# Performance work log

Measured on AMD Instinct MI355X. Metric: run time of the kernel, lower is better.

## Reference

```python
import jax, jax.numpy as jnp
import numpy as np

IGNORE_INDEX = -100
N, C = 2097152, 32


def setup_inputs() -> dict:
    key = jax.random.key(0)
    k1, k2, k3 = jax.random.split(key, 3)
    pred = jax.random.normal(k1, (N, C), dtype=jnp.float32)
    # neg_count (~0.95N) > pos_num * factor (~0.15N).
    r = jax.random.randint(k2, (N,), 0, 100, dtype=jnp.int32)
    cls = jax.random.randint(k3, (N,), 1, C, dtype=jnp.int32)
    label = jnp.where(r >= 95, cls, 0).astype(jnp.int32)
    return {"pred": pred, "label": label, "factor": 3}


def reference(pred, label, factor):
    n = pred.shape[0]
    is_pos = label != 0
    pos_num = jnp.sum(is_pos)
    neg_sum = pos_num * factor
    num_neg = n - pos_num

    # max non-background score per row
    pred_value = jnp.max(pred[:, 1:], axis=1)  # [N]

    # descending sort of negative-position scores (positives pushed to the end)
    neg_scores = jnp.where(is_pos, -jnp.inf, pred_value)
    sorted_desc = -jnp.sort(-neg_scores)
    idx = jnp.clip(neg_sum - 1, 0, n - 1)
    threshold = sorted_desc[idx]

    mask_thr = (pred_value >= threshold) | is_pos
    mask_all = label != -1
    mask = jnp.where(num_neg > neg_sum, mask_thr, mask_all)
    mask = jax.lax.stop_gradient(mask)  # torch computes mask on detached numpy

    masked_label = jnp.where(mask, label, IGNORE_INDEX)
    valid = masked_label != IGNORE_INDEX
    safe_label = jnp.where(valid, masked_label, 0)

    logp = jax.nn.log_softmax(pred, axis=-1)  # [N, C]
    nll = -jnp.take_along_axis(logp, safe_label[:, None], axis=1)[:, 0]  # [N]
    denom = jnp.maximum(jnp.sum(valid), 1)
    loss = jnp.sum(jnp.where(valid, nll, 0.0)) / denom.astype(pred.dtype)
    return loss
```

## Files before the change

### kernel.cpp

```cpp
#include <hip/hip_runtime.h>

#define IGNORE_INDEX (-100)
#define C_DIM 32

struct Ctrl {
    unsigned hist[4][256];
    unsigned pos_num;
    unsigned prefix;
    unsigned rank;
    unsigned use_thr;
    unsigned cnt;
    unsigned pad;
    double   sum;
};

__global__ void init_kernel(unsigned* c, int words) {
    for (int i = threadIdx.x + blockIdx.x * blockDim.x; i < words;
         i += blockDim.x * gridDim.x)
        c[i] = 0u;
}

__device__ inline void wave_hist_add(unsigned* h, unsigned bucket) {
    unsigned long long todo = __ballot(1);
    while (todo) {
        int leader = (int)__builtin_ctzll(todo);
        unsigned b = __shfl(bucket, leader);
        unsigned long long same = __ballot(bucket == b) & todo;
        if ((int)(threadIdx.x & 63) == leader)
            atomicAdd(&h[b], (unsigned)__popcll(same));
        todo &= ~same;
    }
}

__global__ void __launch_bounds__(256)
row_kernel(const float* __restrict__ pred, const int* __restrict__ label,
           unsigned* __restrict__ keys, float* __restrict__ nll,
           Ctrl* __restrict__ c, int n) {
    __shared__ unsigned h[256];
    for (int i = threadIdx.x; i < 256; i += 256) h[i] = 0u;
    __syncthreads();

    int pos_local = 0;
    const int stride = gridDim.x * blockDim.x;
    for (int row = blockIdx.x * blockDim.x + threadIdx.x; row < n; row += stride) {
        const float4* p = reinterpret_cast<const float4*>(pred) + (size_t)row * 8;
        float r[32];
#pragma unroll
        for (int j = 0; j < 8; ++j) {
            float4 v = p[j];
            r[4 * j + 0] = v.x; r[4 * j + 1] = v.y;
            r[4 * j + 2] = v.z; r[4 * j + 3] = v.w;
        }
        float m_nb = r[1];
#pragma unroll
        for (int j = 2; j < 32; ++j) m_nb = fmaxf(m_nb, r[j]);
        float m_all = fmaxf(m_nb, r[0]);

        float s = 0.f;
#pragma unroll
        for (int j = 0; j < 32; ++j) s += __expf(r[j] - m_all);

        int lab = label[row];
        int sl = lab; if (sl < 0) sl = 0; if (sl > 31) sl = 31;
        float xl = r[0];
#pragma unroll
        for (int j = 1; j < 32; ++j) xl = (j == sl) ? r[j] : xl;

        nll[row] = (m_all + __logf(s)) - xl;

        bool is_pos = (lab != 0);
        pos_local += is_pos ? 1 : 0;

        float ns = is_pos ? -__builtin_inff() : m_nb;
        unsigned u = __float_as_uint(ns);
        unsigned ukey = (u & 0x80000000u) ? ~u : (u | 0x80000000u);
        unsigned dkey = ~ukey;
        keys[row] = dkey;
        wave_hist_add(h, dkey >> 24);
    }

#pragma unroll
    for (int off = 32; off > 0; off >>= 1) pos_local += __shfl_down(pos_local, off);
    __shared__ int wsum[4];
    int wid = threadIdx.x >> 6, lane = threadIdx.x & 63;
    if (lane == 0) wsum[wid] = pos_local;
    __syncthreads();
    if (threadIdx.x == 0)
        atomicAdd(&c->pos_num, (unsigned)(wsum[0] + wsum[1] + wsum[2] + wsum[3]));

    for (int i = threadIdx.x; i < 256; i += 256)
        if (h[i]) atomicAdd(&c->hist[3][i], h[i]);
}

__global__ void __launch_bounds__(256)
hist_kernel(const unsigned* __restrict__ keys, Ctrl* __restrict__ c, int n, int pass) {
    __shared__ unsigned h[256];
    for (int i = threadIdx.x; i < 256; i += 256) h[i] = 0u;
    __syncthreads();
    const unsigned prefix = c->prefix;
    const unsigned pmask = 0xFFFFFFFFu << (8 * (pass + 1));
    const int shift = 8 * pass;
    const int stride = gridDim.x * blockDim.x;
    for (int i = blockIdx.x * blockDim.x + threadIdx.x; i < n; i += stride) {
        unsigned k = keys[i];
        if ((k & pmask) == prefix) atomicAdd(&h[(k >> shift) & 0xFFu], 1u);
    }
    __syncthreads();
    for (int i = threadIdx.x; i < 256; i += 256)
        if (h[i]) atomicAdd(&c->hist[pass][i], h[i]);
}

__global__ void scan_kernel(Ctrl* __restrict__ c, const int* __restrict__ factor_p,
                            int pass, int n) {
    __shared__ unsigned s[256];
    __shared__ unsigned sh_rank;
    int t = threadIdx.x;
    if (t == 0) {
        if (pass == 3) {
            long long pos = (long long)c->pos_num;
            long long fac = (long long)factor_p[0];
            long long neg_sum = pos * fac;
            long long num_neg = (long long)n - pos;
            long long idx = neg_sum - 1;
            if (idx < 0) idx = 0;
            if (idx > (long long)n - 1) idx = (long long)n - 1;
            sh_rank = (unsigned)idx;
            c->use_thr = (num_neg > neg_sum) ? 1u : 0u;
        } else {
            sh_rank = c->rank;
        }
    }
    __syncthreads();
    unsigned cnt = c->hist[pass][t];
    s[t] = cnt;
    __syncthreads();
#pragma unroll
    for (int off = 1; off < 256; off <<= 1) {
        unsigned v = (t >= off) ? s[t - off] : 0u;
        __syncthreads();
        s[t] += v;
        __syncthreads();
    }
    unsigned rank = sh_rank;
    unsigned incl = s[t];
    unsigned excl = incl - cnt;
    if (cnt > 0u && excl <= rank && rank < incl) {
        c->prefix |= ((unsigned)t) << (8 * pass);
        c->rank = rank - excl;
    }
}

__global__ void __launch_bounds__(256)
reduce_kernel(const unsigned* __restrict__ keys, const int* __restrict__ label,
              const float* __restrict__ nll, Ctrl* __restrict__ c, int n) {
    const bool use_thr = (c->use_thr != 0u);
    const unsigned thr = c->prefix;
    double local = 0.0;
    int cntl = 0;
    const int stride = gridDim.x * blockDim.x;
    for (int i = blockIdx.x * blockDim.x + threadIdx.x; i < n; i += stride) {
        int lab = label[i];
        bool mask = use_thr ? ((lab != 0) || (keys[i] <= thr)) : (lab != -1);
        if (mask) { local += (double)nll[i]; cntl++; }
    }
#pragma unroll
    for (int off = 32; off > 0; off >>= 1) {
        local += __shfl_down(local, off);
        cntl  += __shfl_down(cntl, off);
    }
    __shared__ double sd[4];
    __shared__ int    si[4];
    int wid = threadIdx.x >> 6, lane = threadIdx.x & 63;
    if (lane == 0) { sd[wid] = local; si[wid] = cntl; }
    __syncthreads();
    if (threadIdx.x == 0) {
        double tot = sd[0] + sd[1] + sd[2] + sd[3];
        int ct = si[0] + si[1] + si[2] + si[3];
        atomicAdd(&c->sum, tot);
        atomicAdd(&c->cnt, (unsigned)ct);
    }
}

__global__ void final_kernel(const Ctrl* __restrict__ c, float* __restrict__ out) {
    if (threadIdx.x == 0 && blockIdx.x == 0) {
        unsigned ct = c->cnt;
        double denom = (ct == 0u) ? 1.0 : (double)ct;
        out[0] = (float)(c->sum / denom);
    }
}

extern "C" void kernel_launch(void* const* d_in, const int* in_sizes, int n_in,
                              void* d_out, int out_size, void* d_ws, size_t ws_size,
                              hipStream_t stream) {
    const float* pred  = (const float*)d_in[0];
    const int* label   = (const int*)d_in[1];
    const int* factor  = (const int*)d_in[2];
    int n = in_sizes[1];
    float* out = (float*)d_out;

    char* ws = (char*)d_ws;
    Ctrl* c = (Ctrl*)ws;
    unsigned* keys = (unsigned*)(ws + 8192);
    float* nll = (float*)(ws + 8192 + (size_t)n * sizeof(unsigned));

    init_kernel<<<1, 256, 0, stream>>>((unsigned*)c, (int)(sizeof(Ctrl) / 4));
    row_kernel<<<2048, 256, 0, stream>>>(pred, label, keys, nll, c, n);
    scan_kernel<<<1, 256, 0, stream>>>(c, factor, 3, n);
    hist_kernel<<<1024, 256, 0, stream>>>(keys, c, n, 2);
    scan_kernel<<<1, 256, 0, stream>>>(c, factor, 2, n);
    hist_kernel<<<1024, 256, 0, stream>>>(keys, c, n, 1);
    scan_kernel<<<1, 256, 0, stream>>>(c, factor, 1, n);
    hist_kernel<<<1024, 256, 0, stream>>>(keys, c, n, 0);
    scan_kernel<<<1, 256, 0, stream>>>(c, factor, 0, n);
    reduce_kernel<<<2048, 256, 0, stream>>>(keys, label, nll, c, n);
    final_kernel<<<1, 64, 0, stream>>>(c, out);
}
```

Baseline: 167.3 us.

## Split each row across 8 lanes and fold scan passes into consumer kernels

The row kernel now assigns one float4 per lane, with 8 lanes per row, and uses shuffles for the max, sum-exp and label gather. This gives fully coalesced loads in place of per-thread 128-byte strided row reads, and cuts register pressure. The four single-block scan kernels are removed: every block of the hist and reduce kernels recomputes the radix-select prefix chain from the global histograms, which drops four launches but repeats the scans redundantly in each block. The histogram atomics now run only on one lane in eight, which leaves most lanes idle during that step.

```diff
diff --git a/kernel.cpp b/kernel.cpp
--- a/kernel.cpp
+++ b/kernel.cpp
@@ -1,16 +1,10 @@
 #include <hip/hip_runtime.h>
 
-#define IGNORE_INDEX (-100)
-#define C_DIM 32
 
 struct Ctrl {
     unsigned hist[4][256];
     unsigned pos_num;
-    unsigned prefix;
-    unsigned rank;
-    unsigned use_thr;
     unsigned cnt;
-    unsigned pad;
     double   sum;
 };
 
@@ -33,57 +27,61 @@
 }
 
 __global__ void __launch_bounds__(256)
-row_kernel(const float* __restrict__ pred, const int* __restrict__ label,
+row_kernel(const float4* __restrict__ pred4, const int* __restrict__ label,
            unsigned* __restrict__ keys, float* __restrict__ nll,
            Ctrl* __restrict__ c, int n) {
     __shared__ unsigned h[256];
     for (int i = threadIdx.x; i < 256; i += 256) h[i] = 0u;
     __syncthreads();
 
+    const int lane  = threadIdx.x & 63;
+    const int sub   = lane & 7;
+    const int gbase = lane & ~7;
+
     int pos_local = 0;
-    const int stride = gridDim.x * blockDim.x;
-    for (int row = blockIdx.x * blockDim.x + threadIdx.x; row < n; row += stride) {
-        const float4* p = reinterpret_cast<const float4*>(pred) + (size_t)row * 8;
-        float r[32];
-#pragma unroll
-        for (int j = 0; j < 8; ++j) {
-            float4 v = p[j];
-            r[4 * j + 0] = v.x; r[4 * j + 1] = v.y;
-            r[4 * j + 2] = v.z; r[4 * j + 3] = v.w;
+    const int rows_per_iter = (gridDim.x * blockDim.x) >> 3;
+    for (int row = (int)((blockIdx.x * blockDim.x + threadIdx.x) >> 3);
+         row < n; row += rows_per_iter) {
+        float4 v = pred4[(size_t)row * 8 + sub];
+
+        float m_nb = (sub == 0) ? fmaxf(fmaxf(v.y, v.z), v.w)
+                                : fmaxf(fmaxf(v.x, v.y), fmaxf(v.z, v.w));
+        m_nb = fmaxf(m_nb, __shfl_xor(m_nb, 1));
+        m_nb = fmaxf(m_nb, __shfl_xor(m_nb, 2));
+        m_nb = fmaxf(m_nb, __shfl_xor(m_nb, 4));
+        float r0    = __shfl(v.x, gbase);
+        float m_all = fmaxf(m_nb, r0);
+
+        float s = __expf(v.x - m_all) + __expf(v.y - m_all)
+                + __expf(v.z - m_all) + __expf(v.w - m_all);
+        s += __shfl_xor(s, 1);
+        s += __shfl_xor(s, 2);
+        s += __shfl_xor(s, 4);
+
+        int lab = label[row];
+        int sl = lab; sl = sl < 0 ? 0 : sl; sl = sl > 31 ? 31 : sl;
+        float cand = (sl & 2) ? ((sl & 1) ? v.w : v.z)
+                              : ((sl & 1) ? v.y : v.x);
+        float xl = __shfl(cand, gbase | (sl >> 2));
+
+        if (sub == 0) {
+            nll[row] = (m_all + __logf(s)) - xl;
+            bool is_pos = (lab != 0);
+            pos_local += is_pos ? 1 : 0;
+            float ns = is_pos ? -__builtin_inff() : m_nb;
+            unsigned u    = __float_as_uint(ns);
+            unsigned ukey = (u & 0x80000000u) ? ~u : (u | 0x80000000u);
+            unsigned dkey = ~ukey;
+            keys[row] = dkey;
+            wave_hist_add(h, dkey >> 24);
         }
-        float m_nb = r[1];
-#pragma unroll
-        for (int j = 2; j < 32; ++j) m_nb = fmaxf(m_nb, r[j]);
-        float m_all = fmaxf(m_nb, r[0]);
-
-        float s = 0.f;
-#pragma unroll
-        for (int j = 0; j < 32; ++j) s += __expf(r[j] - m_all);
-
-        int lab = label[row];
-        int sl = lab; if (sl < 0) sl = 0; if (sl > 31) sl = 31;
-        float xl = r[0];
-#pragma unroll
-        for (int j = 1; j < 32; ++j) xl = (j == sl) ? r[j] : xl;
-
-        nll[row] = (m_all + __logf(s)) - xl;
-
-        bool is_pos = (lab != 0);
-        pos_local += is_pos ? 1 : 0;
-
-        float ns = is_pos ? -__builtin_inff() : m_nb;
-        unsigned u = __float_as_uint(ns);
-        unsigned ukey = (u & 0x80000000u) ? ~u : (u | 0x80000000u);
-        unsigned dkey = ~ukey;
-        keys[row] = dkey;
-        wave_hist_add(h, dkey >> 24);
     }
 
 #pragma unroll
     for (int off = 32; off > 0; off >>= 1) pos_local += __shfl_down(pos_local, off);
     __shared__ int wsum[4];
-    int wid = threadIdx.x >> 6, lane = threadIdx.x & 63;
-    if (lane == 0) wsum[wid] = pos_local;
+    int wid = threadIdx.x >> 6;
+    if ((threadIdx.x & 63) == 0) wsum[wid] = pos_local;
     __syncthreads();
     if (threadIdx.x == 0)
         atomicAdd(&c->pos_num, (unsigned)(wsum[0] + wsum[1] + wsum[2] + wsum[3]));
@@ -92,12 +90,59 @@
         if (h[i]) atomicAdd(&c->hist[3][i], h[i]);
 }
 
+__device__ void select_chain(const Ctrl* __restrict__ c, int n, int factor,
+                             int upto_pass, unsigned& prefix_out,
+                             unsigned& rank_out, bool& use_thr_out) {
+    __shared__ unsigned s[256];
+    __shared__ unsigned sh_byte, sh_rank;
+    const int t = threadIdx.x;
+
+    long long pos     = (long long)c->pos_num;
+    long long neg_sum = pos * (long long)factor;
+    long long num_neg = (long long)n - pos;
+    long long idx     = neg_sum - 1;
+    if (idx < 0) idx = 0;
+    if (idx > (long long)n - 1) idx = (long long)n - 1;
+    unsigned rank   = (unsigned)idx;
+    unsigned prefix = 0u;
+
+    for (int p = 3; p >= upto_pass; --p) {
+        unsigned cnt = c->hist[p][t];
+        __syncthreads();
+        s[t] = cnt;
+        __syncthreads();
+#pragma unroll
+        for (int off = 1; off < 256; off <<= 1) {
+            unsigned v = (t >= off) ? s[t - off] : 0u;
+            __syncthreads();
+            s[t] += v;
+            __syncthreads();
+        }
+        unsigned incl = s[t], excl = incl - cnt;
+        if (cnt > 0u && excl <= rank && rank < incl) {
+            sh_byte = (unsigned)t;
+            sh_rank = rank - excl;
+        }
+        __syncthreads();
+        prefix |= sh_byte << (8 * p);
+        rank = sh_rank;
+        __syncthreads();
+    }
+    prefix_out  = prefix;
+    rank_out    = rank;
+    use_thr_out = (num_neg > neg_sum);
+}
+
 __global__ void __launch_bounds__(256)
-hist_kernel(const unsigned* __restrict__ keys, Ctrl* __restrict__ c, int n, int pass) {
+hist_kernel(const unsigned* __restrict__ keys, Ctrl* __restrict__ c,
+            const int* __restrict__ factor_p, int n, int pass) {
+    unsigned prefix, rank; bool use_thr;
+    select_chain(c, n, factor_p[0], pass + 1, prefix, rank, use_thr);
+
     __shared__ unsigned h[256];
     for (int i = threadIdx.x; i < 256; i += 256) h[i] = 0u;
     __syncthreads();
-    const unsigned prefix = c->prefix;
+
     const unsigned pmask = 0xFFFFFFFFu << (8 * (pass + 1));
     const int shift = 8 * pass;
     const int stride = gridDim.x * blockDim.x;
@@ -110,51 +155,13 @@
         if (h[i]) atomicAdd(&c->hist[pass][i], h[i]);
 }
 
-__global__ void scan_kernel(Ctrl* __restrict__ c, const int* __restrict__ factor_p,
-                            int pass, int n) {
-    __shared__ unsigned s[256];
-    __shared__ unsigned sh_rank;
-    int t = threadIdx.x;
-    if (t == 0) {
-        if (pass == 3) {
-            long long pos = (long long)c->pos_num;
-            long long fac = (long long)factor_p[0];
-            long long neg_sum = pos * fac;
-            long long num_neg = (long long)n - pos;
-            long long idx = neg_sum - 1;
-            if (idx < 0) idx = 0;
-            if (idx > (long long)n - 1) idx = (long long)n - 1;
-            sh_rank = (unsigned)idx;
-            c->use_thr = (num_neg > neg_sum) ? 1u : 0u;
-        } else {
-            sh_rank = c->rank;
-        }
-    }
-    __syncthreads();
-    unsigned cnt = c->hist[pass][t];
-    s[t] = cnt;
-    __syncthreads();
-#pragma unroll
-    for (int off = 1; off < 256; off <<= 1) {
-        unsigned v = (t >= off) ? s[t - off] : 0u;
-        __syncthreads();
-        s[t] += v;
-        __syncthreads();
-    }
-    unsigned rank = sh_rank;
-    unsigned incl = s[t];
-    unsigned excl = incl - cnt;
-    if (cnt > 0u && excl <= rank && rank < incl) {
-        c->prefix |= ((unsigned)t) << (8 * pass);
-        c->rank = rank - excl;
-    }
-}
-
 __global__ void __launch_bounds__(256)
 reduce_kernel(const unsigned* __restrict__ keys, const int* __restrict__ label,
-              const float* __restrict__ nll, Ctrl* __restrict__ c, int n) {
-    const bool use_thr = (c->use_thr != 0u);
-    const unsigned thr = c->prefix;
+              const float* __restrict__ nll, Ctrl* __restrict__ c,
+              const int* __restrict__ factor_p, int n) {
+    unsigned thr, rank; bool use_thr;
+    select_chain(c, n, factor_p[0], 0, thr, rank, use_thr);
+
     double local = 0.0;
     int cntl = 0;
     const int stride = gridDim.x * blockDim.x;
@@ -170,14 +177,12 @@
     }
     __shared__ double sd[4];
     __shared__ int    si[4];
-    int wid = threadIdx.x >> 6, lane = threadIdx.x & 63;
-    if (lane == 0) { sd[wid] = local; si[wid] = cntl; }
+    int wid = threadIdx.x >> 6;
+    if ((threadIdx.x & 63) == 0) { sd[wid] = local; si[wid] = cntl; }
     __syncthreads();
     if (threadIdx.x == 0) {
-        double tot = sd[0] + sd[1] + sd[2] + sd[3];
-        int ct = si[0] + si[1] + si[2] + si[3];
-        atomicAdd(&c->sum, tot);
-        atomicAdd(&c->cnt, (unsigned)ct);
+        atomicAdd(&c->sum, sd[0] + sd[1] + sd[2] + sd[3]);
+        atomicAdd(&c->cnt, (unsigned)(si[0] + si[1] + si[2] + si[3]));
     }
 }
 
@@ -192,9 +197,9 @@
 extern "C" void kernel_launch(void* const* d_in, const int* in_sizes, int n_in,
                               void* d_out, int out_size, void* d_ws, size_t ws_size,
                               hipStream_t stream) {
-    const float* pred  = (const float*)d_in[0];
-    const int* label   = (const int*)d_in[1];
-    const int* factor  = (const int*)d_in[2];
+    const float* pred = (const float*)d_in[0];
+    const int* label  = (const int*)d_in[1];
+    const int* factor = (const int*)d_in[2];
     int n = in_sizes[1];
     float* out = (float*)d_out;
 
@@ -204,14 +209,10 @@
     float* nll = (float*)(ws + 8192 + (size_t)n * sizeof(unsigned));
 
     init_kernel<<<1, 256, 0, stream>>>((unsigned*)c, (int)(sizeof(Ctrl) / 4));
-    row_kernel<<<2048, 256, 0, stream>>>(pred, label, keys, nll, c, n);
-    scan_kernel<<<1, 256, 0, stream>>>(c, factor, 3, n);
-    hist_kernel<<<1024, 256, 0, stream>>>(keys, c, n, 2);
-    scan_kernel<<<1, 256, 0, stream>>>(c, factor, 2, n);
-    hist_kernel<<<1024, 256, 0, stream>>>(keys, c, n, 1);
-    scan_kernel<<<1, 256, 0, stream>>>(c, factor, 1, n);
-    hist_kernel<<<1024, 256, 0, stream>>>(keys, c, n, 0);
-    scan_kernel<<<1, 256, 0, stream>>>(c, factor, 0, n);
-    reduce_kernel<<<2048, 256, 0, stream>>>(keys, label, nll, c, n);
+    row_kernel<<<2048, 256, 0, stream>>>((const float4*)pred, label, keys, nll, c, n);
+    hist_kernel<<<1024, 256, 0, stream>>>(keys, c, factor, n, 2);
+    hist_kernel<<<1024, 256, 0, stream>>>(keys, c, factor, n, 1);
+    hist_kernel<<<1024, 256, 0, stream>>>(keys, c, factor, n, 0);
+    reduce_kernel<<<2048, 256, 0, stream>>>(keys, label, nll, c, factor, n);
     final_kernel<<<1, 64, 0, stream>>>(c, out);
 }
```

Measured after the change: 188.4 us. +12.7%, slower.
